# Performance work log

Hardware: AMD Instinct MI355X
Metric: run time of the kernel (lower is better)

## Reference

```python
import jax, jax.numpy as jnp
import numpy as np

NUM_GRIDS = 8
GRID_MIN, GRID_MAX = -2.0, 2.0
DENOM = (GRID_MAX - GRID_MIN) / (NUM_GRIDS - 1)
GRID = jnp.linspace(GRID_MIN, GRID_MAX, NUM_GRIDS, dtype=jnp.float32)

Q_DIM = K_DIM = V_DIM = 256
HEAD_DIM, NUM_HEADS = 32, 8
TOTAL = HEAD_DIM * NUM_HEADS  # 256
B, S = 128, 8192


def fastkan(x, spline_w, base_w, base_b):
    # RBF expansion: [N, in, G] (layernorm in original is built but never applied)
    basis = jnp.exp(-(((x[..., None] - GRID) / DENOM) ** 2))
    ret = basis.reshape(x.shape[0], -1) @ spline_w          # [N, out]
    base = jax.nn.silu(x) @ base_w + base_b                 # [N, out]
    return ret + base


def setup_inputs() -> dict:
    key = jax.random.key(0)
    ks = jax.random.split(key, 20)
    d = {
        "q": jax.random.normal(ks[0], (B, Q_DIM), jnp.float32),
        "k": jax.random.normal(ks[1], (S, K_DIM), jnp.float32),
        "v": jax.random.normal(ks[2], (S, V_DIM), jnp.float32),
    }
    i = 3
    for name, din, dout in (("q", Q_DIM, TOTAL), ("k", K_DIM, TOTAL), ("v", V_DIM, TOTAL), ("g", Q_DIM, TOTAL), ("o", TOTAL, Q_DIM)):
        d[f"{name}_sw"] = jax.random.truncated_normal(ks[i], -2.0, 2.0, (din * NUM_GRIDS, dout), jnp.float32) * 0.1
        d[f"{name}_bw"] = jax.random.normal(ks[i + 1], (din, dout), jnp.float32) * (1.0 / np.sqrt(din))
        d[f"{name}_bb"] = jnp.zeros((dout,), jnp.float32)
        i += 2
    return d


def reference(q, k, v,
              q_sw, q_bw, q_bb,
              k_sw, k_bw, k_bb,
              v_sw, v_bw, v_bb,
              g_sw, g_bw, g_bb,
              o_sw, o_bw, o_bb):
    norm = 1.0 / np.sqrt(HEAD_DIM)
    wq = (fastkan(q, q_sw, q_bw, q_bb) * norm).reshape(B, NUM_HEADS, HEAD_DIM)   # [B,H,D]
    wk = fastkan(k, k_sw, k_bw, k_bb).reshape(S, NUM_HEADS, HEAD_DIM)            # [S,H,D]
    # broadcast-multiply + reduce == einsum; softmax over key axis S
    att = jax.nn.softmax(jnp.einsum("bhd,shd->bsh", wq, wk), axis=1)             # [B,S,H]
    wv = fastkan(v, v_sw, v_bw, v_bb).reshape(S, NUM_HEADS, HEAD_DIM)            # [S,H,D]
    o = jnp.einsum("bsh,shd->bhd", att, wv).reshape(B, TOTAL)                    # [B,H*D]
    g = jax.nn.sigmoid(fastkan(q, g_sw, g_bw, g_bb))                             # [B,H*D]
    o = g * o
    return fastkan(o, o_sw, o_bw, o_bb)                                          # [B,q_dim]
```

## Files before the change

### kernel.cpp

```cpp
#include <hip/hip_runtime.h>
#include <math.h>

#define IN_DIM 256
#define OUT_DIM 256

typedef short short8 __attribute__((ext_vector_type(8)));
typedef short short4_t __attribute__((ext_vector_type(4)));
typedef float f32x4 __attribute__((ext_vector_type(4)));
typedef unsigned int u32;

static __device__ __forceinline__ short f2bf(float f) {
    union { float f; unsigned u; } c; c.f = f;
    unsigned r = (c.u + 0x7FFFu + ((c.u >> 16) & 1u)) >> 16;
    return (short)r;
}

static __device__ __forceinline__ void gload16(const void* g, void* l) {
    __builtin_amdgcn_global_load_lds(
        (const __attribute__((address_space(1))) u32*)g,
        (__attribute__((address_space(3))) u32*)l, 16, 0, 0);
}

template<int RT, int CT, int MODE>
__global__ __launch_bounds__(256) void fastkan_kernel(
    const float* __restrict__ X, const float* __restrict__ SW,
    const float* __restrict__ BW, const float* __restrict__ BB,
    float* __restrict__ OUT)
{
    constexpr int TRT = RT / 16;
    constexpr int TCT = CT / 16;
    __shared__ float aT[64][RT];
    __shared__ float bT[64][CT];
    const int t = threadIdx.x, tr = t >> 4, tc = t & 15;
    const int r0 = blockIdx.x * RT, c0 = blockIdx.y * CT;
    float acc[TRT][TCT];
#pragma unroll
    for (int a = 0; a < TRT; ++a)
#pragma unroll
        for (int b = 0; b < TCT; ++b) acc[a][b] = 0.f;

    for (int i0 = 0; i0 < IN_DIM; i0 += 8) {
        __syncthreads();
        constexpr int PER_A = (RT * 8) / 256;
#pragma unroll
        for (int j = 0; j < PER_A; ++j) {
            int p = j * 256 + t;
            int i = p & 7, r = p >> 3;
            float x = X[(size_t)(r0 + r) * IN_DIM + (i0 + i)];
#pragma unroll
            for (int g = 0; g < 8; ++g) {
                float z = (x - (-2.0f + (float)g * (4.0f / 7.0f))) * 1.75f;
                aT[i * 8 + g][r] = __expf(-z * z);
            }
        }
#pragma unroll
        for (int j = 0; j < (64 * CT) / 1024; ++j) {
            int p = j * 256 + t;
            int c4 = p % (CT / 4), kk = p / (CT / 4);
            *(float4*)&bT[kk][c4 * 4] =
                *(const float4*)&SW[(size_t)(i0 * 8 + kk) * OUT_DIM + (c0 + c4 * 4)];
        }
        __syncthreads();
#pragma unroll 8
        for (int kk = 0; kk < 64; ++kk) {
            float av[TRT], bv[TCT];
#pragma unroll
            for (int a = 0; a < TRT; ++a) av[a] = aT[kk][tr * TRT + a];
#pragma unroll
            for (int b = 0; b < TCT; ++b) bv[b] = bT[kk][tc * TCT + b];
#pragma unroll
            for (int a = 0; a < TRT; ++a)
#pragma unroll
                for (int b = 0; b < TCT; ++b)
                    acc[a][b] = fmaf(av[a], bv[b], acc[a][b]);
        }
    }
    for (int i0 = 0; i0 < IN_DIM; i0 += 64) {
        __syncthreads();
#pragma unroll
        for (int j = 0; j < (RT * 64) / 1024; ++j) {
            int p = j * 256 + t;
            int i4 = p & 15, r = p >> 4;
            float4 xv = *(const float4*)&X[(size_t)(r0 + r) * IN_DIM + (i0 + i4 * 4)];
            const float* xe = &xv.x;
#pragma unroll
            for (int e = 0; e < 4; ++e) {
                float x = xe[e];
                aT[i4 * 4 + e][r] = x / (1.f + __expf(-x));
            }
        }
#pragma unroll
        for (int j = 0; j < (64 * CT) / 1024; ++j) {
            int p = j * 256 + t;
            int c4 = p % (CT / 4), kk = p / (CT / 4);
            *(float4*)&bT[kk][c4 * 4] =
                *(const float4*)&BW[(size_t)(i0 + kk) * OUT_DIM + (c0 + c4 * 4)];
        }
        __syncthreads();
#pragma unroll 8
        for (int kk = 0; kk < 64; ++kk) {
            float av[TRT], bv[TCT];
#pragma unroll
            for (int a = 0; a < TRT; ++a) av[a] = aT[kk][tr * TRT + a];
#pragma unroll
            for (int b = 0; b < TCT; ++b) bv[b] = bT[kk][tc * TCT + b];
#pragma unroll
            for (int a = 0; a < TRT; ++a)
#pragma unroll
                for (int b = 0; b < TCT; ++b)
                    acc[a][b] = fmaf(av[a], bv[b], acc[a][b]);
        }
    }
#pragma unroll
    for (int a = 0; a < TRT; ++a) {
        int r = r0 + tr * TRT + a;
#pragma unroll
        for (int b = 0; b < TCT; ++b) {
            int c = c0 + tc * TCT + b;
            float v = acc[a][b] + BB[c];
            if (MODE == 1) v *= 0.17677669529663687f;
            if (MODE == 2) v = 1.f / (1.f + __expf(-v));
            OUT[(size_t)r * OUT_DIM + c] = v;
        }
    }
}

__global__ __launch_bounds__(256) void fastkan_splitk(
    const float* __restrict__ X,
    const float* __restrict__ SW0, const float* __restrict__ BW0,
    const float* __restrict__ SW1, const float* __restrict__ BW1,
    float* __restrict__ PART)
{
    __shared__ float aT[128][65];
    __shared__ float bT[64][33];

    const int t = threadIdx.x;
    const int tr = t >> 4, tc = t & 15;
    const int c0 = blockIdx.x * 32;
    const int kc = blockIdx.y;
    const int z = blockIdx.z;
    const float* SW = z ? SW1 : SW0;
    const float* BW = z ? BW1 : BW0;

    float acc[8][2];
#pragma unroll
    for (int a = 0; a < 8; ++a) { acc[a][0] = 0.f; acc[a][1] = 0.f; }

    for (int sub = 0; sub < 4; ++sub) {
        const int k0 = kc * 256 + sub * 64;
        __syncthreads();
        if (kc < 8) {
            const int i0 = kc * 32 + sub * 8;
#pragma unroll
            for (int it = 0; it < 4; ++it) {
                int p = it * 256 + t;
                int row = p & 127, i = p >> 7;
                float x = X[(size_t)row * 256 + i0 + i];
#pragma unroll
                for (int g = 0; g < 8; ++g) {
                    float zz = (x - (-2.0f + (float)g * (4.0f / 7.0f))) * 1.75f;
                    aT[row][i * 8 + g] = __expf(-zz * zz);
                }
            }
        } else {
            const int f0 = sub * 64;
            int row = t >> 1, seg = t & 1;
            const float* xr = &X[(size_t)row * 256 + f0 + seg * 32];
#pragma unroll
            for (int j4 = 0; j4 < 8; ++j4) {
                float4 xv = *(const float4*)&xr[j4 * 4];
                const float* xe = &xv.x;
#pragma unroll
                for (int e = 0; e < 4; ++e) {
                    float x = xe[e];
                    aT[row][seg * 32 + j4 * 4 + e] = x / (1.f + __expf(-x));
                }
            }
        }
        {
            const float* Wsrc = (kc < 8) ? &SW[(size_t)k0 * 256] : &BW[(size_t)(k0 - 2048) * 256];
#pragma unroll
            for (int it = 0; it < 2; ++it) {
                int p = it * 256 + t;
                int kk = p >> 3, c4 = p & 7;
                float4 v = *(const float4*)&Wsrc[(size_t)kk * 256 + c0 + c4 * 4];
                bT[kk][c4 * 4 + 0] = v.x; bT[kk][c4 * 4 + 1] = v.y;
                bT[kk][c4 * 4 + 2] = v.z; bT[kk][c4 * 4 + 3] = v.w;
            }
        }
        __syncthreads();
#pragma unroll 8
        for (int kk = 0; kk < 64; ++kk) {
            float av[8], bv[2];
#pragma unroll
            for (int a = 0; a < 8; ++a) av[a] = aT[tr * 8 + a][kk];
            bv[0] = bT[kk][tc * 2 + 0];
            bv[1] = bT[kk][tc * 2 + 1];
#pragma unroll
            for (int a = 0; a < 8; ++a) {
                acc[a][0] = fmaf(av[a], bv[0], acc[a][0]);
                acc[a][1] = fmaf(av[a], bv[1], acc[a][1]);
            }
        }
    }
#pragma unroll
    for (int a = 0; a < 8; ++a) {
        int r = tr * 8 + a;
        float* dst = &PART[((size_t)(z * 9 + kc) * 128 + r) * 256 + c0 + tc * 2];
        dst[0] = acc[a][0];
        dst[1] = acc[a][1];
    }
}

template<int MODE>
__global__ __launch_bounds__(256) void reduce_kernel(
    const float* __restrict__ PART, const float* __restrict__ BB, float* __restrict__ OUT)
{
    const int r = blockIdx.x, t = threadIdx.x;
    float s = 0.f;
#pragma unroll
    for (int kc = 0; kc < 9; ++kc)
        s += PART[((size_t)kc * 128 + r) * 256 + t];
    float v = s + BB[t];
    if (MODE == 1) v *= 0.17677669529663687f;
    if (MODE == 2) v = 1.f / (1.f + __expf(-v));
    OUT[(size_t)r * 256 + t] = v;
}

template<int WB>
__global__ __launch_bounds__(256) void reduce_qg(
    const float* __restrict__ PART, const float* __restrict__ QBB,
    const float* __restrict__ GBB, float* __restrict__ WQ, float* __restrict__ GB,
    short* __restrict__ WQb)
{
    const int r = blockIdx.x, t = threadIdx.x, z = blockIdx.y;
    const float* P = PART + (size_t)z * 9 * 128 * 256;
    float s = 0.f;
#pragma unroll
    for (int kc = 0; kc < 9; ++kc)
        s += P[((size_t)kc * 128 + r) * 256 + t];
    if (z == 0) {
        float v = (s + QBB[t]) * 0.17677669529663687f;
        WQ[(size_t)r * 256 + t] = v;
        if (WB) WQb[(size_t)r * 256 + t] = f2bf(v);
    } else {
        float v = s + GBB[t];
        GB[(size_t)r * 256 + t] = 1.f / (1.f + __expf(-v));
    }
}

__global__ __launch_bounds__(256) void prep_kernel(
    const float* __restrict__ SWk, const float* __restrict__ BWk, short* __restrict__ Bk,
    const float* __restrict__ SWv, const float* __restrict__ BWv, short* __restrict__ Bv)
{
    __shared__ float tile[64][65];
    const int t = threadIdx.x;
    const int kk0 = blockIdx.x * 64;
    const int c0 = blockIdx.y * 64;
    const float* SW = blockIdx.z ? SWv : SWk;
    const float* BW = blockIdx.z ? BWv : BWk;
    short* Bdst = blockIdx.z ? Bv : Bk;

#pragma unroll
    for (int j = 0; j < 4; ++j) {
        int p = j * 256 + t;
        int lr = p >> 4, lc4 = p & 15;
        float4 v;
        if (kk0 < 2048) v = *(const float4*)&SW[(size_t)(kk0 + lr) * 256 + c0 + lc4 * 4];
        else            v = *(const float4*)&BW[(size_t)(kk0 - 2048 + lr) * 256 + c0 + lc4 * 4];
        tile[lr][lc4 * 4 + 0] = v.x; tile[lr][lc4 * 4 + 1] = v.y;
        tile[lr][lc4 * 4 + 2] = v.z; tile[lr][lc4 * 4 + 3] = v.w;
    }
    __syncthreads();
#pragma unroll
    for (int j = 0; j < 4; ++j) {
        int p = j * 256 + t;
        int lc = p >> 4, lk4 = p & 15;
        short4_t s;
#pragma unroll
        for (int e = 0; e < 4; ++e) s[e] = f2bf(tile[lk4 * 4 + e][lc]);
        *(short4_t*)&Bdst[(size_t)(c0 + lc) * 2304 + kk0 + lk4 * 4] = s;
    }
}

__global__ __launch_bounds__(256) void basis_gen2(
    const float* __restrict__ K, const float* __restrict__ V,
    short* __restrict__ A0, short* __restrict__ A1)
{
    const float* X = blockIdx.y ? V : K;
    short* A = blockIdx.y ? A1 : A0;
    const int row = blockIdx.x;
    const int t = threadIdx.x;
    float x = X[(size_t)row * 256 + t];
    short8 s;
#pragma unroll
    for (int g = 0; g < 8; ++g) {
        float z = (x - (-2.0f + (float)g * (4.0f / 7.0f))) * 1.75f;
        s[g] = f2bf(__expf(-z * z));
    }
    *(short8*)&A[(size_t)row * 2304 + t * 8] = s;
    if (t < 32) {
        const float* xr = &X[(size_t)row * 256 + t * 8];
        short8 sl;
#pragma unroll
        for (int e2 = 0; e2 < 2; ++e2) {
            float4 xv = *(const float4*)&xr[e2 * 4];
            const float* xe = &xv.x;
#pragma unroll
            for (int e = 0; e < 4; ++e) {
                float xx = xe[e];
                sl[e2 * 4 + e] = f2bf(xx / (1.f + __expf(-xx)));
            }
        }
        *(short8*)&A[(size_t)row * 2304 + 2048 + t * 8] = sl;
    }
}

__global__ __launch_bounds__(256) void prep_basis(
    const float* __restrict__ K, const float* __restrict__ V,
    short* __restrict__ A0, short* __restrict__ A1,
    const float* __restrict__ SWk, const float* __restrict__ BWk, short* __restrict__ Bk,
    const float* __restrict__ SWv, const float* __restrict__ BWv, short* __restrict__ Bv)
{
    __shared__ float tile[64][65];
    const int bid = blockIdx.x;
    const int t = threadIdx.x;
    if (bid < 16384) {
        const float* X = (bid >> 13) ? V : K;
        short* A = (bid >> 13) ? A1 : A0;
        const int row = bid & 8191;
        float x = X[(size_t)row * 256 + t];
        short8 s;
#pragma unroll
        for (int g = 0; g < 8; ++g) {
            float z = (x - (-2.0f + (float)g * (4.0f / 7.0f))) * 1.75f;
            s[g] = f2bf(__expf(-z * z));
        }
        *(short8*)&A[(size_t)row * 2304 + t * 8] = s;
        if (t < 32) {
            const float* xr = &X[(size_t)row * 256 + t * 8];
            short8 sl;
#pragma unroll
            for (int e2 = 0; e2 < 2; ++e2) {
                float4 xv = *(const float4*)&xr[e2 * 4];
                const float* xe = &xv.x;
#pragma unroll
                for (int e = 0; e < 4; ++e) {
                    float xx = xe[e];
                    sl[e2 * 4 + e] = f2bf(xx / (1.f + __expf(-xx)));
                }
            }
            *(short8*)&A[(size_t)row * 2304 + 2048 + t * 8] = sl;
        }
        return;
    }
    const int p = bid - 16384;
    const int zz = p / 144;
    const int q = p % 144;
    const int kk0 = (q >> 2) * 64;
    const int c0 = (q & 3) * 64;
    const float* SW = zz ? SWv : SWk;
    const float* BW = zz ? BWv : BWk;
    short* Bdst = zz ? Bv : Bk;

#pragma unroll
    for (int j = 0; j < 4; ++j) {
        int pp = j * 256 + t;
        int lr = pp >> 4, lc4 = pp & 15;
        float4 v;
        if (kk0 < 2048) v = *(const float4*)&SW[(size_t)(kk0 + lr) * 256 + c0 + lc4 * 4];
        else            v = *(const float4*)&BW[(size_t)(kk0 - 2048 + lr) * 256 + c0 + lc4 * 4];
        tile[lr][lc4 * 4 + 0] = v.x; tile[lr][lc4 * 4 + 1] = v.y;
        tile[lr][lc4 * 4 + 2] = v.z; tile[lr][lc4 * 4 + 3] = v.w;
    }
    __syncthreads();
#pragma unroll
    for (int j = 0; j < 4; ++j) {
        int pp = j * 256 + t;
        int lc = pp >> 4, lk4 = pp & 15;
        short4_t s;
#pragma unroll
        for (int e = 0; e < 4; ++e) s[e] = f2bf(tile[lk4 * 4 + e][lc]);
        *(short4_t*)&Bdst[(size_t)(c0 + lc) * 2304 + kk0 + lk4 * 4] = s;
    }
}

__global__ __launch_bounds__(256) void stage2(
    const short* __restrict__ A0, const short* __restrict__ A1,
    const short* __restrict__ Bk, const short* __restrict__ Bv,
    const float* __restrict__ BBk, const float* __restrict__ BBv,
    short* __restrict__ WKb, short* __restrict__ WVb,
    const float* __restrict__ PART, const float* __restrict__ QBB,
    const float* __restrict__ GBB, float* __restrict__ GB,
    short* __restrict__ WQb)
{
    __shared__ __align__(16) short Al[128 * 64];
    __shared__ __align__(16) short Bl[64 * 64];

    const int bid = blockIdx.x;
    const int t = threadIdx.x;

    if (bid >= 512) {
        const int p = bid - 512;
        const int r = p % 128, z = p / 128;
        const float* P = PART + (size_t)z * 9 * 128 * 256;
        float s = 0.f;
#pragma unroll
        for (int kc = 0; kc < 9; ++kc)
            s += P[((size_t)kc * 128 + r) * 256 + t];
        if (z == 0) {
            WQb[(size_t)r * 256 + t] = f2bf((s + QBB[t]) * 0.17677669529663687f);
        } else {
            float v = s + GBB[t];
            GB[(size_t)r * 256 + t] = 1.f / (1.f + __expf(-v));
        }
        return;
    }

    const int x = bid & 63;
    const int y = (bid >> 6) & 3;
    const int z = bid >> 8;
    const short* A  = z ? A1 : A0;
    const short* B2 = z ? Bv : Bk;
    const float* BB = z ? BBv : BBk;
    short* OUT      = z ? WVb : WKb;

    const int r0 = x * 128;
    const int c0 = y * 64;
    const int lane = t & 63, wid = t >> 6;
    const int wm = wid >> 1, wn = wid & 1;
    const int lrow = lane & 15;
    const int lkb = (lane >> 4) * 16;

    f32x4 acc[4][2];
#pragma unroll
    for (int a = 0; a < 4; ++a)
#pragma unroll
        for (int c = 0; c < 2; ++c) acc[a][c] = (f32x4){0.f, 0.f, 0.f, 0.f};

    for (int st = 0; st < 36; ++st) {
        const int k0 = st * 64;
        __syncthreads();
#pragma unroll
        for (int i = 0; i < 4; ++i) {
            int f = i * 256 + t;
            int row = f >> 3, kg = f & 7;
            gload16(&A[(size_t)(r0 + row) * 2304 + k0 + kg * 8], (char*)Al + f * 16);
        }
#pragma unroll
        for (int i = 0; i < 2; ++i) {
            int f = i * 256 + t;
            int c = f >> 3, kg = f & 7;
            gload16(&B2[(size_t)(c0 + c) * 2304 + k0 + kg * 8], (char*)Bl + f * 16);
        }
        __syncthreads();
#pragma unroll
        for (int kf = 0; kf < 2; ++kf) {
            short8 af[4], bf[2];
#pragma unroll
            for (int a = 0; a < 4; ++a) {
                int R = wm * 64 + a * 16 + lrow;
                af[a] = *(short8*)((char*)Al + R * 128 + kf * 64 + lkb);
            }
#pragma unroll
            for (int c = 0; c < 2; ++c) {
                int R = wn * 32 + c * 16 + lrow;
                bf[c] = *(short8*)((char*)Bl + R * 128 + kf * 64 + lkb);
            }
#pragma unroll
            for (int a = 0; a < 4; ++a)
#pragma unroll
                for (int c = 0; c < 2; ++c)
                    acc[a][c] = __builtin_amdgcn_mfma_f32_16x16x32_bf16(af[a], bf[c], acc[a][c], 0, 0, 0);
        }
    }
#pragma unroll
    for (int a = 0; a < 4; ++a)
#pragma unroll
        for (int c = 0; c < 2; ++c) {
            int col = c0 + wn * 32 + c * 16 + lrow;
            float bias = BB[col];
#pragma unroll
            for (int j = 0; j < 4; ++j) {
                int row = r0 + wm * 64 + a * 16 + (lane >> 4) * 4 + j;
                OUT[(size_t)row * 256 + col] = f2bf(acc[a][c][j] + bias);
            }
        }
}

__global__ __launch_bounds__(256) void gemm_tile(
    const short* __restrict__ A, const short* __restrict__ B2,
    const float* __restrict__ BB, float* __restrict__ OUT)
{
    __shared__ __align__(16) short A_l[64 * 64];
    __shared__ __align__(16) short B_l[64 * 64];
    char* ab = (char*)A_l;
    char* bb = (char*)B_l;

    const int t = threadIdx.x;
    const int r0 = blockIdx.x * 64;
    const int c0 = blockIdx.y * 64;
    const int lane = t & 63;
    const int wid = t >> 6;
    const int wm = wid >> 1, wn = wid & 1;
    const int lrow = lane & 15;
    const int lkb = (lane >> 4) * 16;

    f32x4 acc[2][2];
#pragma unroll
    for (int a = 0; a < 2; ++a)
#pragma unroll
        for (int c = 0; c < 2; ++c) acc[a][c] = (f32x4){0.f, 0.f, 0.f, 0.f};

    for (int st = 0; st < 36; ++st) {
        const int k0 = st * 64;
        __syncthreads();
#pragma unroll
        for (int it = 0; it < 2; ++it) {
            int p = it * 256 + t;
            int row = p >> 3, kg = p & 7;
            short8 s = *(const short8*)&A[(size_t)(r0 + row) * 2304 + k0 + kg * 8];
            int off = (row * 128 + kg * 16) ^ ((row & 7) << 4);
            *(short8*)(ab + off) = s;
        }
#pragma unroll
        for (int it = 0; it < 2; ++it) {
            int p = it * 256 + t;
            int c = p >> 3, kg = p & 7;
            short8 s = *(const short8*)&B2[(size_t)(c0 + c) * 2304 + k0 + kg * 8];
            int off = (c * 128 + kg * 16) ^ ((c & 7) << 4);
            *(short8*)(bb + off) = s;
        }
        __syncthreads();
#pragma unroll
        for (int kf = 0; kf < 2; ++kf) {
            short8 af[2], bf[2];
#pragma unroll
            for (int a = 0; a < 2; ++a) {
                int R = wm * 32 + a * 16 + lrow;
                int off = (R * 128 + kf * 64 + lkb) ^ ((R & 7) << 4);
                af[a] = *(short8*)(ab + off);
            }
#pragma unroll
            for (int c = 0; c < 2; ++c) {
                int R = wn * 32 + c * 16 + lrow;
                int off = (R * 128 + kf * 64 + lkb) ^ ((R & 7) << 4);
                bf[c] = *(short8*)(bb + off);
            }
#pragma unroll
            for (int a = 0; a < 2; ++a)
#pragma unroll
                for (int c = 0; c < 2; ++c)
                    acc[a][c] = __builtin_amdgcn_mfma_f32_16x16x32_bf16(af[a], bf[c], acc[a][c], 0, 0, 0);
        }
    }
#pragma unroll
    for (int a = 0; a < 2; ++a)
#pragma unroll
        for (int c = 0; c < 2; ++c) {
            int col = c0 + wn * 32 + c * 16 + (lane & 15);
            float bias = BB[col];
#pragma unroll
            for (int j = 0; j < 4; ++j) {
                int row = r0 + wm * 32 + a * 16 + (lane >> 4) * 4 + j;
                OUT[(size_t)row * 256 + col] = acc[a][c][j] + bias;
            }
        }
}

__global__ __launch_bounds__(256) void attn_mfma(
    const short* __restrict__ WQb, const short* __restrict__ WKb, const short* __restrict__ WVb,
    float* __restrict__ OPART, float* __restrict__ LPART)
{
    __shared__ __align__(16) short Ql[128 * 32];
    __shared__ __align__(16) short Kl[64 * 32];
    __shared__ __align__(16) short Vt[32 * 64];
    __shared__ __align__(16) short El[128 * 64];
    char* ql = (char*)Ql; char* kl = (char*)Kl;
    char* vt = (char*)Vt; char* el = (char*)El;

    const int t = threadIdx.x, lane = t & 63, w = t >> 6;
    const int ch = blockIdx.x, h = blockIdx.y, s0 = ch * 64;
    const int lr = lane & 15, lg = lane >> 4;

    {
        int f = t;
        gload16(&WQb[(size_t)(f >> 2) * 256 + h * 32 + (f & 3) * 8], ql + f * 16);
        f = t + 256;
        gload16(&WQb[(size_t)(f >> 2) * 256 + h * 32 + (f & 3) * 8], ql + f * 16);
        gload16(&WKb[(size_t)(s0 + (t >> 2)) * 256 + h * 32 + (t & 3) * 8], kl + t * 16);
        int s = t >> 2, d8 = (t & 3) * 8;
        short8 vv = *(const short8*)&WVb[(size_t)(s0 + s) * 256 + h * 32 + d8];
#pragma unroll
        for (int e = 0; e < 8; ++e) {
            int d = d8 + e;
            *(short*)(vt + ((d * 128 + s * 2) ^ ((d & 7) << 4))) = vv[e];
        }
    }
    __syncthreads();

#pragma unroll
    for (int i = 0; i < 2; ++i) {
        const int q = (w * 2 + i) * 16 + lr;
        short8 bq = *(short8*)(ql + q * 64 + lg * 16);
        float ls = 0.f;
#pragma unroll
        for (int j = 0; j < 4; ++j) {
            short8 ak = *(short8*)(kl + (j * 16 + lr) * 64 + lg * 16);
            f32x4 sc = {0.f, 0.f, 0.f, 0.f};
            sc = __builtin_amdgcn_mfma_f32_16x16x32_bf16(ak, bq, sc, 0, 0, 0);
            short4_t ep;
#pragma unroll
            for (int jj = 0; jj < 4; ++jj) {
                float e = __expf(sc[jj] - 16.0f);
                ls += e;
                ep[jj] = f2bf(e);
            }
            int sb = j * 16 + lg * 4;
            *(short4_t*)(el + ((q * 128 + sb * 2) ^ ((q & 7) << 4))) = ep;
        }
        ls += __shfl_xor(ls, 16);
        ls += __shfl_xor(ls, 32);
        if (lg == 0)
            LPART[(size_t)(ch * 8 + h) * 128 + (w * 2 + i) * 16 + lr] = ls;
    }
    __syncthreads();

    f32x4 oacc[2][2];
#pragma unroll
    for (int i = 0; i < 2; ++i)
#pragma unroll
        for (int d = 0; d < 2; ++d) oacc[i][d] = (f32x4){0.f, 0.f, 0.f, 0.f};
#pragma unroll
    for (int kf = 0; kf < 2; ++kf) {
        short8 ea[2], vb[2];
#pragma unroll
        for (int i = 0; i < 2; ++i) {
            int q = (w * 2 + i) * 16 + lr;
            ea[i] = *(short8*)(el + ((q * 128 + kf * 64 + lg * 16) ^ ((q & 7) << 4)));
        }
#pragma unroll
        for (int d = 0; d < 2; ++d) {
            int dd = d * 16 + lr;
            vb[d] = *(short8*)(vt + ((dd * 128 + kf * 64 + lg * 16) ^ ((dd & 7) << 4)));
        }
#pragma unroll
        for (int i = 0; i < 2; ++i)
#pragma unroll
            for (int d = 0; d < 2; ++d)
                oacc[i][d] = __builtin_amdgcn_mfma_f32_16x16x32_bf16(ea[i], vb[d], oacc[i][d], 0, 0, 0);
    }
#pragma unroll
    for (int i = 0; i < 2; ++i)
#pragma unroll
        for (int d = 0; d < 2; ++d) {
            int dd = d * 16 + lr;
#pragma unroll
            for (int j = 0; j < 4; ++j) {
                int q = (w * 2 + i) * 16 + lg * 4 + j;
                OPART[((size_t)(ch * 8 + h) * 128 + q) * 32 + dd] = oacc[i][d][j];
            }
        }
}

__global__ __launch_bounds__(256) void attn_reduce2(
    const float* __restrict__ OPART, const float* __restrict__ LPART,
    const float* __restrict__ G, float* __restrict__ OMID)
{
    __shared__ float so[8][33];
    __shared__ float sl[8];
    const int b = blockIdx.x, h = blockIdx.y;
    const int t = threadIdx.x;
    const int d = t & 31, part = t >> 5;
    float o = 0.f, l = 0.f;
#pragma unroll 4
    for (int cc = 0; cc < 16; ++cc) {
        int ch = part * 16 + cc;
        o += OPART[((size_t)(ch * 8 + h) * 128 + b) * 32 + d];
        l += LPART[(size_t)(ch * 8 + h) * 128 + b];
    }
    so[part][d] = o;
    if (d == 0) sl[part] = l;
    __syncthreads();
    if (t < 32) {
        float oo = 0.f, ll = 0.f;
#pragma unroll
        for (int p = 0; p < 8; ++p) { oo += so[p][t]; ll += sl[p]; }
        int idx = b * 256 + h * 32 + t;
        OMID[idx] = G[idx] * (oo / ll);
    }
}

__global__ __launch_bounds__(256) void attn_chunk(
    const float* __restrict__ WQ, const float* __restrict__ WK, const float* __restrict__ WV,
    float* __restrict__ OPART, float* __restrict__ LPART)
{
    __shared__ float sWQ[128][33];
    __shared__ float sWK[64][33];
    __shared__ float sWV[64][33];
    __shared__ float sE[128][66];
    __shared__ float lred[128][16];

    const int t = threadIdx.x;
    const int ch = blockIdx.x;
    const int h = blockIdx.y;
    const int s0 = ch * 64;

    {
        int b = t >> 1, seg = t & 1;
        const float* src = &WQ[(size_t)b * 256 + h * 32 + seg * 16];
#pragma unroll
        for (int j = 0; j < 4; ++j) {
            float4 v = *(const float4*)&src[j * 4];
            sWQ[b][seg * 16 + j * 4 + 0] = v.x; sWQ[b][seg * 16 + j * 4 + 1] = v.y;
            sWQ[b][seg * 16 + j * 4 + 2] = v.z; sWQ[b][seg * 16 + j * 4 + 3] = v.w;
        }
        if (t < 128) {
            int s = t >> 1; seg = t & 1;
            const float* sk = &WK[(size_t)(s0 + s) * 256 + h * 32 + seg * 16];
#pragma unroll
            for (int j = 0; j < 4; ++j) {
                float4 v = *(const float4*)&sk[j * 4];
                sWK[s][seg * 16 + j * 4 + 0] = v.x; sWK[s][seg * 16 + j * 4 + 1] = v.y;
                sWK[s][seg * 16 + j * 4 + 2] = v.z; sWK[s][seg * 16 + j * 4 + 3] = v.w;
            }
        } else {
            int t2 = t - 128;
            int s = t2 >> 1; seg = t2 & 1;
            const float* sv = &WV[(size_t)(s0 + s) * 256 + h * 32 + seg * 16];
#pragma unroll
            for (int j = 0; j < 4; ++j) {
                float4 v = *(const float4*)&sv[j * 4];
                sWV[s][seg * 16 + j * 4 + 0] = v.x; sWV[s][seg * 16 + j * 4 + 1] = v.y;
                sWV[s][seg * 16 + j * 4 + 2] = v.z; sWV[s][seg * 16 + j * 4 + 3] = v.w;
            }
        }
    }
    __syncthreads();

    const int tr = t >> 4, tc = t & 15;
    {
        float acc[8][4];
#pragma unroll
        for (int a = 0; a < 8; ++a)
#pragma unroll
            for (int b = 0; b < 4; ++b) acc[a][b] = 0.f;
#pragma unroll 4
        for (int kk = 0; kk < 32; ++kk) {
            float av[8], bv[4];
#pragma unroll
            for (int a = 0; a < 8; ++a) av[a] = sWQ[tr * 8 + a][kk];
#pragma unroll
            for (int b = 0; b < 4; ++b) bv[b] = sWK[tc * 4 + b][kk];
#pragma unroll
            for (int a = 0; a < 8; ++a)
#pragma unroll
                for (int b = 0; b < 4; ++b) acc[a][b] = fmaf(av[a], bv[b], acc[a][b]);
        }
#pragma unroll
        for (int a = 0; a < 8; ++a) {
            float lp = 0.f;
#pragma unroll
            for (int b = 0; b < 4; ++b) {
                float e = __expf(acc[a][b] - 16.0f);
                sE[tr * 8 + a][tc * 4 + b] = e;
                lp += e;
            }
            lred[tr * 8 + a][tc] = lp;
        }
    }
    __syncthreads();
    if (t < 128) {
        float l = 0.f;
#pragma unroll
        for (int j = 0; j < 16; ++j) l += lred[t][j];
        LPART[(size_t)(ch * 8 + h) * 128 + t] = l;
    }

    {
        float acc2[8][2];
#pragma unroll
        for (int a = 0; a < 8; ++a) { acc2[a][0] = 0.f; acc2[a][1] = 0.f; }
#pragma unroll 4
        for (int kk = 0; kk < 64; ++kk) {
            float av[8], bv[2];
#pragma unroll
            for (int a = 0; a < 8; ++a) av[a] = sE[tr * 8 + a][kk];
            bv[0] = sWV[kk][tc * 2 + 0];
            bv[1] = sWV[kk][tc * 2 + 1];
#pragma unroll
            for (int a = 0; a < 8; ++a) {
                acc2[a][0] = fmaf(av[a], bv[0], acc2[a][0]);
                acc2[a][1] = fmaf(av[a], bv[1], acc2[a][1]);
            }
        }
#pragma unroll
        for (int a = 0; a < 8; ++a) {
            int b = tr * 8 + a;
            float* dst = &OPART[((size_t)(ch * 8 + h) * 128 + b) * 32 + tc * 2];
            dst[0] = acc2[a][0];
            dst[1] = acc2[a][1];
        }
    }
}

__global__ __launch_bounds__(256) void attn_reduce(
    const float* __restrict__ OPART, const float* __restrict__ LPART,
    const float* __restrict__ G, float* __restrict__ OMID)
{
    const int b = blockIdx.x;
    const int t = threadIdx.x;
    const int h = t >> 5, d = t & 31;
    float o = 0.f, l = 0.f;
    for (int ch = 0; ch < 128; ++ch) {
        o += OPART[((size_t)(ch * 8 + h) * 128 + b) * 32 + d];
        l += LPART[(size_t)(ch * 8 + h) * 128 + b];
    }
    int idx = b * 256 + h * 32 + d;
    OMID[idx] = G[idx] * (o / l);
}

__global__ __launch_bounds__(256) void attn_kernel(
    const float* __restrict__ WQ, const float* __restrict__ WK, const float* __restrict__ WV,
    const float* __restrict__ G, float* __restrict__ OMID)
{
    __shared__ float red[4][64][33];
    const int h = blockIdx.y;
    const int bl = threadIdx.x >> 6;
    const int lane = threadIdx.x & 63;
    const int b = blockIdx.x * 4 + bl;
    float q[32];
    {
        const float* wq = &WQ[(size_t)b * 256 + h * 32];
#pragma unroll
        for (int j = 0; j < 8; ++j) {
            float4 v = *(const float4*)&wq[j * 4];
            q[j * 4 + 0] = v.x; q[j * 4 + 1] = v.y; q[j * 4 + 2] = v.z; q[j * 4 + 3] = v.w;
        }
    }
    float o[32];
#pragma unroll
    for (int d = 0; d < 32; ++d) o[d] = 0.f;
    float l = 0.f;
#pragma unroll 2
    for (int s = lane; s < 8192; s += 64) {
        const float* kr = &WK[(size_t)s * 256 + h * 32];
        float s0 = 0, s1 = 0, s2 = 0, s3 = 0;
#pragma unroll
        for (int j = 0; j < 8; ++j) {
            float4 kv = *(const float4*)&kr[j * 4];
            s0 = fmaf(q[j * 4 + 0], kv.x, s0);
            s1 = fmaf(q[j * 4 + 1], kv.y, s1);
            s2 = fmaf(q[j * 4 + 2], kv.z, s2);
            s3 = fmaf(q[j * 4 + 3], kv.w, s3);
        }
        float e = __expf((s0 + s1) + (s2 + s3) - 16.0f);
        l += e;
        const float* vr = &WV[(size_t)s * 256 + h * 32];
#pragma unroll
        for (int j = 0; j < 8; ++j) {
            float4 vv = *(const float4*)&vr[j * 4];
            o[j * 4 + 0] = fmaf(e, vv.x, o[j * 4 + 0]);
            o[j * 4 + 1] = fmaf(e, vv.y, o[j * 4 + 1]);
            o[j * 4 + 2] = fmaf(e, vv.z, o[j * 4 + 2]);
            o[j * 4 + 3] = fmaf(e, vv.w, o[j * 4 + 3]);
        }
    }
#pragma unroll
    for (int d = 0; d < 32; ++d) red[bl][lane][d] = o[d];
    red[bl][lane][32] = l;
    __syncthreads();
    if (threadIdx.x < 128) {
        int bl2 = threadIdx.x >> 5;
        int d = threadIdx.x & 31;
        float os = 0.f, ls = 0.f;
#pragma unroll 8
        for (int ln = 0; ln < 64; ++ln) {
            os += red[bl2][ln][d];
            ls += red[bl2][ln][32];
        }
        int b2 = blockIdx.x * 4 + bl2;
        int idx = b2 * 256 + h * 32 + d;
        OMID[idx] = G[idx] * (os / ls);
    }
}

extern "C" void kernel_launch(void* const* d_in, const int* in_sizes, int n_in,
                              void* d_out, int out_size, void* d_ws, size_t ws_size,
                              hipStream_t stream) {
    const float* q    = (const float*)d_in[0];
    const float* k    = (const float*)d_in[1];
    const float* v    = (const float*)d_in[2];
    const float* q_sw = (const float*)d_in[3];
    const float* q_bw = (const float*)d_in[4];
    const float* q_bb = (const float*)d_in[5];
    const float* k_sw = (const float*)d_in[6];
    const float* k_bw = (const float*)d_in[7];
    const float* k_bb = (const float*)d_in[8];
    const float* v_sw = (const float*)d_in[9];
    const float* v_bw = (const float*)d_in[10];
    const float* v_bb = (const float*)d_in[11];
    const float* g_sw = (const float*)d_in[12];
    const float* g_bw = (const float*)d_in[13];
    const float* g_bb = (const float*)d_in[14];
    const float* o_sw = (const float*)d_in[15];
    const float* o_bw = (const float*)d_in[16];
    const float* o_bb = (const float*)d_in[17];

    float* ws = (float*)d_ws;
    float* wk = ws;
    float* wv = ws + 2097152;
    float* wq = ws + 4194304;
    float* gb = ws + 4227072;
    float* om = ws + 4259840;
    short* Bk = (short*)(ws + 4292608);
    short* Bv = (short*)(ws + 4587520);
    float* Opart = ws + 4882432;
    float* Lpart = ws + 9076736;
    float* PART = Opart;
    short* A0 = (short*)(ws + 9207808);
    short* A1 = (short*)(ws + 18644992);
    short* WKb = (short*)(ws + 28082176);
    short* WVb = (short*)(ws + 29130752);
    short* WQb = (short*)(ws + 30179328);
    short* Abuf = (short*)Opart;
    float* out = (float*)d_out;

    const bool can_mfma   = ws_size >= (size_t)4882432 * 4;
    const bool can_bigger = ws_size >= (size_t)(4882432 + 9437184) * 4;
    const bool can_huge   = ws_size >= (size_t)30195712 * 4;

    dim3 blk(256);
    if (can_huge) {
        prep_basis<<<dim3(16672), blk, 0, stream>>>(k, v, A0, A1,
                                                    k_sw, k_bw, Bk, v_sw, v_bw, Bv);
        fastkan_splitk<<<dim3(8, 9, 2), blk, 0, stream>>>(q, q_sw, q_bw, g_sw, g_bw, PART);
        stage2<<<dim3(768), blk, 0, stream>>>(A0, A1, Bk, Bv, k_bb, v_bb, WKb, WVb,
                                              PART, q_bb, g_bb, gb, WQb);
        attn_mfma<<<dim3(128, 8), blk, 0, stream>>>(WQb, WKb, WVb, Opart, Lpart);
        attn_reduce2<<<dim3(128, 8), blk, 0, stream>>>(Opart, Lpart, gb, om);
        fastkan_splitk<<<dim3(8, 9, 1), blk, 0, stream>>>(om, o_sw, o_bw, o_sw, o_bw, PART);
        reduce_kernel<0><<<dim3(128), blk, 0, stream>>>(PART, o_bb, out);
    } else if (can_bigger) {
        prep_kernel<<<dim3(36, 4, 2), blk, 0, stream>>>(k_sw, k_bw, Bk, v_sw, v_bw, Bv);
        fastkan_splitk<<<dim3(8, 9, 2), blk, 0, stream>>>(q, q_sw, q_bw, g_sw, g_bw, PART);
        reduce_qg<0><<<dim3(128, 2), blk, 0, stream>>>(PART, q_bb, g_bb, wq, gb, (short*)wq);
        basis_gen2<<<dim3(8192, 1), blk, 0, stream>>>(k, k, Abuf, Abuf);
        gemm_tile<<<dim3(128, 4), blk, 0, stream>>>(Abuf, Bk, k_bb, wk);
        basis_gen2<<<dim3(8192, 1), blk, 0, stream>>>(v, v, Abuf, Abuf);
        gemm_tile<<<dim3(128, 4), blk, 0, stream>>>(Abuf, Bv, v_bb, wv);
        attn_chunk<<<dim3(128, 8), blk, 0, stream>>>(wq, wk, wv, Opart, Lpart);
        attn_reduce<<<dim3(128), blk, 0, stream>>>(Opart, Lpart, gb, om);
        fastkan_splitk<<<dim3(8, 9, 1), blk, 0, stream>>>(om, o_sw, o_bw, o_sw, o_bw, PART);
        reduce_kernel<0><<<dim3(128), blk, 0, stream>>>(PART, o_bb, out);
    } else {
        fastkan_kernel<64, 64, 0><<<dim3(128, 4), blk, 0, stream>>>(k, k_sw, k_bw, k_bb, wk);
        fastkan_kernel<64, 64, 0><<<dim3(128, 4), blk, 0, stream>>>(v, v_sw, v_bw, v_bb, wv);
        fastkan_kernel<32, 32, 1><<<dim3(4, 8), blk, 0, stream>>>(q, q_sw, q_bw, q_bb, wq);
        fastkan_kernel<32, 32, 2><<<dim3(4, 8), blk, 0, stream>>>(q, g_sw, g_bw, g_bb, gb);
        attn_kernel<<<dim3(32, 8), blk, 0, stream>>>(wq, wk, wv, gb, om);
        fastkan_kernel<32, 32, 0><<<dim3(4, 8), blk, 0, stream>>>(om, o_sw, o_bw, o_bb, out);
    }
}
```

Before: 116.0 us.

## Split stage2 K/V GEMM along K with larger 128x128 tiles, sum halves in attention

```diff
diff --git a/kernel.cpp b/kernel.cpp
--- a/kernel.cpp
+++ b/kernel.cpp
@@ -13,6 +13,11 @@
     union { float f; unsigned u; } c; c.f = f;
     unsigned r = (c.u + 0x7FFFu + ((c.u >> 16) & 1u)) >> 16;
     return (short)r;
+}
+static __device__ __forceinline__ float bf2f(short s) {
+    union { unsigned u; float f; } c;
+    c.u = ((u32)(unsigned short)s) << 16;
+    return c.f;
 }
 
 static __device__ __forceinline__ void gload16(const void* g, void* l) {
@@ -389,13 +394,14 @@
     const short* __restrict__ A0, const short* __restrict__ A1,
     const short* __restrict__ Bk, const short* __restrict__ Bv,
     const float* __restrict__ BBk, const float* __restrict__ BBv,
-    short* __restrict__ WKb, short* __restrict__ WVb,
+    short* __restrict__ GPk0, short* __restrict__ GPk1,
+    short* __restrict__ GPv0, short* __restrict__ GPv1,
     const float* __restrict__ PART, const float* __restrict__ QBB,
     const float* __restrict__ GBB, float* __restrict__ GB,
     short* __restrict__ WQb)
 {
     __shared__ __align__(16) short Al[128 * 64];
-    __shared__ __align__(16) short Bl[64 * 64];
+    __shared__ __align__(16) short Bl[128 * 64];
 
     const int bid = blockIdx.x;
     const int t = threadIdx.x;
@@ -418,28 +424,30 @@
     }
 
     const int x = bid & 63;
-    const int y = (bid >> 6) & 3;
-    const int z = bid >> 8;
-    const short* A  = z ? A1 : A0;
-    const short* B2 = z ? Bv : Bk;
-    const float* BB = z ? BBv : BBk;
-    short* OUT      = z ? WVb : WKb;
+    const int y = (bid >> 6) & 1;
+    const int z = bid >> 7;
+    const int mat = z >> 1, kh = z & 1;
+    const short* A  = mat ? A1 : A0;
+    const short* B2 = mat ? Bv : Bk;
+    const float* BB = mat ? BBv : BBk;
+    short* OUT = mat ? (kh ? GPv1 : GPv0) : (kh ? GPk1 : GPk0);
 
     const int r0 = x * 128;
-    const int c0 = y * 64;
+    const int c0 = y * 128;
+    const int kbase = kh * 1152;
     const int lane = t & 63, wid = t >> 6;
     const int wm = wid >> 1, wn = wid & 1;
     const int lrow = lane & 15;
     const int lkb = (lane >> 4) * 16;
 
-    f32x4 acc[4][2];
+    f32x4 acc[4][4];
 #pragma unroll
     for (int a = 0; a < 4; ++a)
 #pragma unroll
-        for (int c = 0; c < 2; ++c) acc[a][c] = (f32x4){0.f, 0.f, 0.f, 0.f};
-
-    for (int st = 0; st < 36; ++st) {
-        const int k0 = st * 64;
+        for (int c = 0; c < 4; ++c) acc[a][c] = (f32x4){0.f, 0.f, 0.f, 0.f};
+
+    for (int st = 0; st < 18; ++st) {
+        const int k0 = kbase + st * 64;
         __syncthreads();
 #pragma unroll
         for (int i = 0; i < 4; ++i) {
@@ -448,7 +456,7 @@
             gload16(&A[(size_t)(r0 + row) * 2304 + k0 + kg * 8], (char*)Al + f * 16);
         }
 #pragma unroll
-        for (int i = 0; i < 2; ++i) {
+        for (int i = 0; i < 4; ++i) {
             int f = i * 256 + t;
             int c = f >> 3, kg = f & 7;
             gload16(&B2[(size_t)(c0 + c) * 2304 + k0 + kg * 8], (char*)Bl + f * 16);
@@ -456,30 +464,30 @@
         __syncthreads();
 #pragma unroll
         for (int kf = 0; kf < 2; ++kf) {
-            short8 af[4], bf[2];
+            short8 af[4], bf[4];
 #pragma unroll
             for (int a = 0; a < 4; ++a) {
                 int R = wm * 64 + a * 16 + lrow;
                 af[a] = *(short8*)((char*)Al + R * 128 + kf * 64 + lkb);
             }
 #pragma unroll
-            for (int c = 0; c < 2; ++c) {
-                int R = wn * 32 + c * 16 + lrow;
-                bf[c] = *(short8*)((char*)Bl + R * 128 + kf * 64 + lkb);
+            for (int c = 0; c < 4; ++c) {
+                int C = wn * 64 + c * 16 + lrow;
+                bf[c] = *(short8*)((char*)Bl + C * 128 + kf * 64 + lkb);
             }
 #pragma unroll
             for (int a = 0; a < 4; ++a)
 #pragma unroll
-                for (int c = 0; c < 2; ++c)
+                for (int c = 0; c < 4; ++c)
                     acc[a][c] = __builtin_amdgcn_mfma_f32_16x16x32_bf16(af[a], bf[c], acc[a][c], 0, 0, 0);
         }
     }
 #pragma unroll
     for (int a = 0; a < 4; ++a)
 #pragma unroll
-        for (int c = 0; c < 2; ++c) {
-            int col = c0 + wn * 32 + c * 16 + lrow;
-            float bias = BB[col];
+        for (int c = 0; c < 4; ++c) {
+            int col = c0 + wn * 64 + c * 16 + lrow;
+            float bias = (kh == 0) ? BB[col] : 0.f;
 #pragma unroll
             for (int j = 0; j < 4; ++j) {
                 int row = r0 + wm * 64 + a * 16 + (lane >> 4) * 4 + j;
@@ -569,7 +577,9 @@
 }
 
 __global__ __launch_bounds__(256) void attn_mfma(
-    const short* __restrict__ WQb, const short* __restrict__ WKb, const short* __restrict__ WVb,
+    const short* __restrict__ WQb,
+    const short* __restrict__ K0, const short* __restrict__ K1,
+    const short* __restrict__ V0, const short* __restrict__ V1,
     float* __restrict__ OPART, float* __restrict__ LPART)
 {
     __shared__ __align__(16) short Ql[128 * 32];
@@ -588,13 +598,20 @@
         gload16(&WQb[(size_t)(f >> 2) * 256 + h * 32 + (f & 3) * 8], ql + f * 16);
         f = t + 256;
         gload16(&WQb[(size_t)(f >> 2) * 256 + h * 32 + (f & 3) * 8], ql + f * 16);
-        gload16(&WKb[(size_t)(s0 + (t >> 2)) * 256 + h * 32 + (t & 3) * 8], kl + t * 16);
         int s = t >> 2, d8 = (t & 3) * 8;
-        short8 vv = *(const short8*)&WVb[(size_t)(s0 + s) * 256 + h * 32 + d8];
+        size_t off = (size_t)(s0 + s) * 256 + h * 32 + d8;
+        short8 ka = *(const short8*)&K0[off];
+        short8 kb = *(const short8*)&K1[off];
+        short8 ks;
+#pragma unroll
+        for (int e = 0; e < 8; ++e) ks[e] = f2bf(bf2f(ka[e]) + bf2f(kb[e]));
+        *(short8*)(kl + t * 16) = ks;
+        short8 va = *(const short8*)&V0[off];
+        short8 vb = *(const short8*)&V1[off];
 #pragma unroll
         for (int e = 0; e < 8; ++e) {
             int d = d8 + e;
-            *(short*)(vt + ((d * 128 + s * 2) ^ ((d & 7) << 4))) = vv[e];
+            *(short*)(vt + ((d * 128 + s * 2) ^ ((d & 7) << 4))) = f2bf(bf2f(va[e]) + bf2f(vb[e]));
         }
     }
     __syncthreads();
@@ -920,24 +937,27 @@
     float* PART = Opart;
     short* A0 = (short*)(ws + 9207808);
     short* A1 = (short*)(ws + 18644992);
-    short* WKb = (short*)(ws + 28082176);
-    short* WVb = (short*)(ws + 29130752);
-    short* WQb = (short*)(ws + 30179328);
+    short* GPk0 = (short*)(ws + 28082176);
+    short* GPk1 = (short*)(ws + 29130752);
+    short* GPv0 = (short*)(ws + 30179328);
+    short* GPv1 = (short*)(ws + 31227904);
+    short* WQb  = (short*)(ws + 32276480);
     short* Abuf = (short*)Opart;
     float* out = (float*)d_out;
 
     const bool can_mfma   = ws_size >= (size_t)4882432 * 4;
     const bool can_bigger = ws_size >= (size_t)(4882432 + 9437184) * 4;
-    const bool can_huge   = ws_size >= (size_t)30195712 * 4;
+    const bool can_huge   = ws_size >= (size_t)32292864 * 4;
 
     dim3 blk(256);
     if (can_huge) {
         prep_basis<<<dim3(16672), blk, 0, stream>>>(k, v, A0, A1,
                                                     k_sw, k_bw, Bk, v_sw, v_bw, Bv);
         fastkan_splitk<<<dim3(8, 9, 2), blk, 0, stream>>>(q, q_sw, q_bw, g_sw, g_bw, PART);
-        stage2<<<dim3(768), blk, 0, stream>>>(A0, A1, Bk, Bv, k_bb, v_bb, WKb, WVb,
+        stage2<<<dim3(768), blk, 0, stream>>>(A0, A1, Bk, Bv, k_bb, v_bb,
+                                              GPk0, GPk1, GPv0, GPv1,
                                               PART, q_bb, g_bb, gb, WQb);
-        attn_mfma<<<dim3(128, 8), blk, 0, stream>>>(WQb, WKb, WVb, Opart, Lpart);
+        attn_mfma<<<dim3(128, 8), blk, 0, stream>>>(WQb, GPk0, GPk1, GPv0, GPv1, Opart, Lpart);
         attn_reduce2<<<dim3(128, 8), blk, 0, stream>>>(Opart, Lpart, gb, om);
         fastkan_splitk<<<dim3(8, 9, 1), blk, 0, stream>>>(om, o_sw, o_bw, o_sw, o_bw, PART);
         reduce_kernel<0><<<dim3(128), blk, 0, stream>>>(PART, o_bb, out);
```

Result: faster. 113.0 us (-2.6%).

## Fold q and gate projections into prep_basis and stage2 bf16 MFMA path

Applied to the files above, without the earlier changes.

```diff
diff --git a/kernel.cpp b/kernel.cpp
--- a/kernel.cpp
+++ b/kernel.cpp
@@ -13,6 +13,11 @@
     union { float f; unsigned u; } c; c.f = f;
     unsigned r = (c.u + 0x7FFFu + ((c.u >> 16) & 1u)) >> 16;
     return (short)r;
+}
+static __device__ __forceinline__ float bf2f(short s) {
+    union { unsigned u; float f; } c;
+    c.u = ((u32)(unsigned short)s) << 16;
+    return c.f;
 }
 
 static __device__ __forceinline__ void gload16(const void* g, void* l) {
@@ -317,17 +322,20 @@
 }
 
 __global__ __launch_bounds__(256) void prep_basis(
-    const float* __restrict__ K, const float* __restrict__ V,
-    short* __restrict__ A0, short* __restrict__ A1,
+    const float* __restrict__ K, const float* __restrict__ V, const float* __restrict__ Q,
+    short* __restrict__ A0, short* __restrict__ A1, short* __restrict__ Aq,
     const float* __restrict__ SWk, const float* __restrict__ BWk, short* __restrict__ Bk,
-    const float* __restrict__ SWv, const float* __restrict__ BWv, short* __restrict__ Bv)
+    const float* __restrict__ SWv, const float* __restrict__ BWv, short* __restrict__ Bv,
+    const float* __restrict__ SWq, const float* __restrict__ BWq, short* __restrict__ Bq,
+    const float* __restrict__ SWg, const float* __restrict__ BWg, short* __restrict__ Bg)
 {
     __shared__ float tile[64][65];
     const int bid = blockIdx.x;
     const int t = threadIdx.x;
-    if (bid < 16384) {
-        const float* X = (bid >> 13) ? V : K;
-        short* A = (bid >> 13) ? A1 : A0;
+    if (bid < 16512) {
+        const int m = bid >> 13;
+        const float* X = (m == 0) ? K : ((m == 1) ? V : Q);
+        short* A = (m == 0) ? A0 : ((m == 1) ? A1 : Aq);
         const int row = bid & 8191;
         float x = X[(size_t)row * 256 + t];
         short8 s;
@@ -354,14 +362,14 @@
         }
         return;
     }
-    const int p = bid - 16384;
-    const int zz = p / 144;
+    const int p = bid - 16512;
+    const int mat = p / 144;
     const int q = p % 144;
     const int kk0 = (q >> 2) * 64;
     const int c0 = (q & 3) * 64;
-    const float* SW = zz ? SWv : SWk;
-    const float* BW = zz ? BWv : BWk;
-    short* Bdst = zz ? Bv : Bk;
+    const float* SW = (mat == 0) ? SWk : ((mat == 1) ? SWv : ((mat == 2) ? SWq : SWg));
+    const float* BW = (mat == 0) ? BWk : ((mat == 1) ? BWv : ((mat == 2) ? BWq : BWg));
+    short* Bdst     = (mat == 0) ? Bk  : ((mat == 1) ? Bv  : ((mat == 2) ? Bq  : Bg));
 
 #pragma unroll
     for (int j = 0; j < 4; ++j) {
@@ -386,52 +394,43 @@
 }
 
 __global__ __launch_bounds__(256) void stage2(
-    const short* __restrict__ A0, const short* __restrict__ A1,
+    const short* __restrict__ A0, const short* __restrict__ A1, const short* __restrict__ Aq,
     const short* __restrict__ Bk, const short* __restrict__ Bv,
+    const short* __restrict__ Bq, const short* __restrict__ Bg,
     const float* __restrict__ BBk, const float* __restrict__ BBv,
+    const float* __restrict__ QBB, const float* __restrict__ GBB,
     short* __restrict__ WKb, short* __restrict__ WVb,
-    const float* __restrict__ PART, const float* __restrict__ QBB,
-    const float* __restrict__ GBB, float* __restrict__ GB,
-    short* __restrict__ WQb)
+    short* __restrict__ WQb, float* __restrict__ GB)
 {
     __shared__ __align__(16) short Al[128 * 64];
     __shared__ __align__(16) short Bl[64 * 64];
 
     const int bid = blockIdx.x;
     const int t = threadIdx.x;
-
-    if (bid >= 512) {
-        const int p = bid - 512;
-        const int r = p % 128, z = p / 128;
-        const float* P = PART + (size_t)z * 9 * 128 * 256;
-        float s = 0.f;
-#pragma unroll
-        for (int kc = 0; kc < 9; ++kc)
-            s += P[((size_t)kc * 128 + r) * 256 + t];
-        if (z == 0) {
-            WQb[(size_t)r * 256 + t] = f2bf((s + QBB[t]) * 0.17677669529663687f);
-        } else {
-            float v = s + GBB[t];
-            GB[(size_t)r * 256 + t] = 1.f / (1.f + __expf(-v));
-        }
-        return;
-    }
-
-    const int x = bid & 63;
-    const int y = (bid >> 6) & 3;
-    const int z = bid >> 8;
-    const short* A  = z ? A1 : A0;
-    const short* B2 = z ? Bv : Bk;
-    const float* BB = z ? BBv : BBk;
-    short* OUT      = z ? WVb : WKb;
-
-    const int r0 = x * 128;
-    const int c0 = y * 64;
     const int lane = t & 63, wid = t >> 6;
     const int wm = wid >> 1, wn = wid & 1;
     const int lrow = lane & 15;
     const int lkb = (lane >> 4) * 16;
 
+    const short* A;
+    const short* B2;
+    int r0, c0, which;
+    if (bid < 512) {
+        which = bid >> 8;
+        const int rem = bid & 255;
+        A  = which ? A1 : A0;
+        B2 = which ? Bv : Bk;
+        r0 = (rem & 63) * 128;
+        c0 = (rem >> 6) * 64;
+    } else {
+        const int p = bid - 512;
+        which = 2 + (p >> 2);
+        A = Aq;
+        B2 = (which == 3) ? Bg : Bq;
+        r0 = 0;
+        c0 = (p & 3) * 64;
+    }
+
     f32x4 acc[4][2];
 #pragma unroll
     for (int a = 0; a < 4; ++a)
@@ -464,8 +463,8 @@
             }
 #pragma unroll
             for (int c = 0; c < 2; ++c) {
-                int R = wn * 32 + c * 16 + lrow;
-                bf[c] = *(short8*)((char*)Bl + R * 128 + kf * 64 + lkb);
+                int C = wn * 32 + c * 16 + lrow;
+                bf[c] = *(short8*)((char*)Bl + C * 128 + kf * 64 + lkb);
             }
 #pragma unroll
             for (int a = 0; a < 4; ++a)
@@ -474,16 +473,26 @@
                     acc[a][c] = __builtin_amdgcn_mfma_f32_16x16x32_bf16(af[a], bf[c], acc[a][c], 0, 0, 0);
         }
     }
+
 #pragma unroll
     for (int a = 0; a < 4; ++a)
 #pragma unroll
         for (int c = 0; c < 2; ++c) {
             int col = c0 + wn * 32 + c * 16 + lrow;
-            float bias = BB[col];
 #pragma unroll
             for (int j = 0; j < 4; ++j) {
                 int row = r0 + wm * 64 + a * 16 + (lane >> 4) * 4 + j;
-                OUT[(size_t)row * 256 + col] = f2bf(acc[a][c][j] + bias);
+                if (which == 0) {
+                    WKb[(size_t)row * 256 + col] = f2bf(acc[a][c][j] + BBk[col]);
+                } else if (which == 1) {
+                    WVb[(size_t)row * 256 + col] = f2bf(acc[a][c][j] + BBv[col]);
+                } else if (which == 2) {
+                    WQb[(size_t)row * 256 + col] =
+                        f2bf((acc[a][c][j] + QBB[col]) * 0.17677669529663687f);
+                } else {
+                    float v = acc[a][c][j] + GBB[col];
+                    GB[(size_t)row * 256 + col] = 1.f / (1.f + __expf(-v));
+                }
             }
         }
 }
@@ -923,20 +932,25 @@
     short* WKb = (short*)(ws + 28082176);
     short* WVb = (short*)(ws + 29130752);
     short* WQb = (short*)(ws + 30179328);
+    short* Bq  = (short*)(ws + 32292864);
+    short* Bg  = (short*)(ws + 32587776);
+    short* Aq  = (short*)(ws + 32882688);
     short* Abuf = (short*)Opart;
     float* out = (float*)d_out;
 
     const bool can_mfma   = ws_size >= (size_t)4882432 * 4;
     const bool can_bigger = ws_size >= (size_t)(4882432 + 9437184) * 4;
-    const bool can_huge   = ws_size >= (size_t)30195712 * 4;
+    const bool can_huge   = ws_size >= (size_t)33095680 * 4;
 
     dim3 blk(256);
     if (can_huge) {
-        prep_basis<<<dim3(16672), blk, 0, stream>>>(k, v, A0, A1,
-                                                    k_sw, k_bw, Bk, v_sw, v_bw, Bv);
-        fastkan_splitk<<<dim3(8, 9, 2), blk, 0, stream>>>(q, q_sw, q_bw, g_sw, g_bw, PART);
-        stage2<<<dim3(768), blk, 0, stream>>>(A0, A1, Bk, Bv, k_bb, v_bb, WKb, WVb,
-                                              PART, q_bb, g_bb, gb, WQb);
+        prep_basis<<<dim3(17088), blk, 0, stream>>>(
+            k, v, q, A0, A1, Aq,
+            k_sw, k_bw, Bk, v_sw, v_bw, Bv,
+            q_sw, q_bw, Bq, g_sw, g_bw, Bg);
+        stage2<<<dim3(520), blk, 0, stream>>>(
+            A0, A1, Aq, Bk, Bv, Bq, Bg, k_bb, v_bb, q_bb, g_bb,
+            WKb, WVb, WQb, gb);
         attn_mfma<<<dim3(128, 8), blk, 0, stream>>>(WQb, WKb, WVb, Opart, Lpart);
         attn_reduce2<<<dim3(128, 8), blk, 0, stream>>>(Opart, Lpart, gb, om);
         fastkan_splitk<<<dim3(8, 9, 1), blk, 0, stream>>>(om, o_sw, o_bw, o_sw, o_bw, PART);
@@ -944,7 +958,7 @@
     } else if (can_bigger) {
         prep_kernel<<<dim3(36, 4, 2), blk, 0, stream>>>(k_sw, k_bw, Bk, v_sw, v_bw, Bv);
         fastkan_splitk<<<dim3(8, 9, 2), blk, 0, stream>>>(q, q_sw, q_bw, g_sw, g_bw, PART);
-        reduce_qg<0><<<dim3(128, 2), blk, 0, stream>>>(PART, q_bb, g_bb, wq, gb, (short*)wq);
+        reduce_qg<0><<<dim3(128, 2), blk, 0, stream>>>(PART, q_bb, g_bb, wq, gb, WQb);
         basis_gen2<<<dim3(8192, 1), blk, 0, stream>>>(k, k, Abuf, Abuf);
         gemm_tile<<<dim3(128, 4), blk, 0, stream>>>(Abuf, Bk, k_bb, wk);
         basis_gen2<<<dim3(8192, 1), blk, 0, stream>>>(v, v, Abuf, Abuf);
```

Result: no change. 115.2 us (-0.7%).
